# Kernel tuning notes

Measured on AMD Instinct MI355X. Metric: run time of the kernel, lower is better.

The kernel has to match this reference:

```python
import jax, jax.numpy as jnp
import numpy as np

B, S, D = 8, 1024, 1024      # batch, seq_len, inp_dim
H, HD = 8, 64                # head_num, head_dim
HID = H * HD                 # hidden_dim = 512
P = 2 * D                    # p_factor * inp_dim = 2048
K = 4                        # causal conv kernel size
EPS = 1e-6
CAP = 15.0                   # soft cap for i/f gates


def _layernorm(x, g, b):
    mu = jnp.mean(x, -1, keepdims=True)
    var = jnp.var(x, -1, keepdims=True)
    return (x - mu) * jax.lax.rsqrt(var + EPS) * g + b


def _soft_cap(v):
    return CAP * jnp.tanh(v / CAP)


def _causal_conv_feat(x, w, b):
    # Conv1d(1,1,K) applied over the FEATURE axis of each timestep (as in the
    # torch code: x_t.unsqueeze(1) -> (bs,1,P)), causal left pad of K-1.
    L = x.shape[-1]
    xp = jnp.pad(x, ((0, 0), (0, 0), (K - 1, 0)))
    out = b
    for m in range(K):
        out = out + w[m] * xp[..., m:m + L]
    return out


def _forward(x, ln_g, ln_b, mh_g, mh_b, W_up_l, b_up_l, W_up_r, b_up_r,
             W_down, b_down, conv_w, conv_b, W_skip, b_skip, W_i, b_i,
             W_f, b_f, W_o, b_o, W_q, b_q, W_k, b_k, W_v, b_v):
    Bs, Sl, _ = x.shape
    xn = _layernorm(x, ln_g, ln_b)
    x_t = xn @ W_up_l.T + b_up_l                      # (B,S,P)
    r_t = xn @ W_up_r.T + b_up_r                      # (B,S,HID)
    x_c = jax.nn.silu(_causal_conv_feat(x_t, conv_w, conv_b))
    x_skip = x_c @ W_skip.T + b_skip                  # (B,S,HID)
    q = (x_c @ W_q.T + b_q).reshape(Bs, Sl, H, HD)
    k = (x_c @ W_k.T + b_k).reshape(Bs, Sl, H, HD) / float(np.sqrt(HD))
    v = (x_t @ W_v.T + b_v).reshape(Bs, Sl, H, HD)
    i_pre = _soft_cap(x_c @ W_i.T + b_i)              # (B,S,H)
    f_pre = _soft_cap(x_c @ W_f.T + b_f)              # (B,S,H)
    o = jax.nn.sigmoid(x_t @ W_o.T + b_o)             # (B,S,HID)

    def step(carry, inp):
        c, n, m = carry
        qt, kt, vt, it, ft = inp
        m_t = jnp.maximum(ft + m, it)
        ie = jnp.exp(it - m_t)
        fe = jnp.exp(ft - m_t + m)
        c = fe[:, :, None, None] * c + ie[:, :, None, None] * jnp.einsum('bhd,bhe->bhde', vt, kt)
        n = fe[:, :, None] * n + ie[:, :, None] * kt
        num = jnp.einsum('bhde,bhe->bhd', c, qt)
        den = jnp.maximum(jnp.sum(n * qt, -1, keepdims=True), 1.0)
        return (c, n, m_t), num / den

    c0 = jnp.zeros((Bs, H, HD, HD), x.dtype)
    n0 = jnp.ones((Bs, H, HD), x.dtype)
    m0 = jnp.zeros((Bs, H), x.dtype)
    seq = tuple(jnp.moveaxis(a, 1, 0) for a in (q, k, v, i_pre, f_pre))
    _, hs = jax.lax.scan(step, (c0, n0, m0), seq)     # hs: (S,B,H,HD)
    h = o * jnp.moveaxis(hs, 0, 1).reshape(Bs, Sl, HID)
    hn = _layernorm(h.reshape(Bs, Sl, H, HD), mh_g, mh_b).reshape(Bs, Sl, HID)
    out = (hn + x_skip) * jax.nn.silu(r_t)
    return out @ W_down.T + b_down + x


def setup_inputs() -> dict:
    key = jax.random.key(0)
    ks = jax.random.split(key, 16)

    def w(kk, shape):
        return jax.random.normal(kk, shape, jnp.float32) / np.sqrt(shape[-1]).astype(np.float32)

    return {
        'x': jax.random.normal(ks[0], (B, S, D), jnp.float32),
        'ln_g': jnp.ones((D,), jnp.float32), 'ln_b': jnp.zeros((D,), jnp.float32),
        'mh_g': jnp.ones((H, HD), jnp.float32), 'mh_b': jnp.zeros((H, HD), jnp.float32),
        'W_up_l': w(ks[1], (P, D)), 'b_up_l': jnp.zeros((P,), jnp.float32),
        'W_up_r': w(ks[2], (HID, D)), 'b_up_r': jnp.zeros((HID,), jnp.float32),
        'W_down': w(ks[3], (D, HID)), 'b_down': jnp.zeros((D,), jnp.float32),
        'conv_w': jax.random.normal(ks[4], (K,), jnp.float32) * 0.3,
        'conv_b': jnp.zeros((), jnp.float32),
        'W_skip': w(ks[5], (HID, P)), 'b_skip': jnp.zeros((HID,), jnp.float32),
        'W_i': w(ks[6], (H, P)), 'b_i': jnp.zeros((H,), jnp.float32),
        'W_f': w(ks[7], (H, P)), 'b_f': jnp.zeros((H,), jnp.float32),
        'W_o': w(ks[8], (HID, P)), 'b_o': jnp.zeros((HID,), jnp.float32),
        'W_q': w(ks[9], (HID, P)), 'b_q': jnp.zeros((HID,), jnp.float32),
        'W_k': w(ks[10], (HID, P)), 'b_k': jnp.zeros((HID,), jnp.float32),
        'W_v': w(ks[11], (HID, P)), 'b_v': jnp.zeros((HID,), jnp.float32),
    }


def reference(x, ln_g, ln_b, mh_g, mh_b, W_up_l, b_up_l, W_up_r, b_up_r,
              W_down, b_down, conv_w, conv_b, W_skip, b_skip, W_i, b_i,
              W_f, b_f, W_o, b_o, W_q, b_q, W_k, b_k, W_v, b_v):
    return _forward(x, ln_g, ln_b, mh_g, mh_b, W_up_l, b_up_l, W_up_r, b_up_r,
                    W_down, b_down, conv_w, conv_b, W_skip, b_skip, W_i, b_i,
                    W_f, b_f, W_o, b_o, W_q, b_q, W_k, b_k, W_v, b_v)
```

## Files before the change

kernel.cpp:

```cpp
#include <hip/hip_runtime.h>
#include <hip/hip_bf16.h>
#include <math.h>

#define Bq 8
#define Sq 1024
#define Dq 1024
#define Hq 8
#define HDq 64
#define HIDq 512
#define Pq 2048
#define EPSq 1e-6f
#define CAPq 15.0f
#define NCq 16
#define CLq 64
#define LDST 40
#define ARENA (128 * LDST)
#define GEMM_SMEM_BYTES (2 * 4 * ARENA * 2)

typedef __attribute__((ext_vector_type(8))) short short8;
typedef __attribute__((ext_vector_type(4))) float f32x4v;
typedef __hip_bfloat16 bf16;

__device__ inline void split2(float v, bf16& h, bf16& l) {
  h = __float2bfloat16(v);
  l = __float2bfloat16(v - __bfloat162float(h));
}

__global__ __launch_bounds__(256) void cvtw_all(
    const float* __restrict__ s0, const float* __restrict__ s1,
    const float* __restrict__ s2, const float* __restrict__ s3,
    const float* __restrict__ s4, const float* __restrict__ s5,
    const float* __restrict__ s6, const float* __restrict__ s7,
    bf16* __restrict__ hi, bf16* __restrict__ lo)
{
  int u = blockIdx.x * 256 + threadIdx.x;
  const float* src; int segBase;
  if      (u <  524288) { src = s0; segBase = 0;       }
  else if (u <  655360) { src = s1; segBase = 524288;  }
  else if (u <  917504) { src = s2; segBase = 655360;  }
  else if (u < 1179648) { src = s3; segBase = 917504;  }
  else if (u < 1441792) { src = s4; segBase = 1179648; }
  else if (u < 1703936) { src = s5; segBase = 1441792; }
  else if (u < 1966080) { src = s6; segBase = 1703936; }
  else                  { src = s7; segBase = 1966080; }
  float4 v = ((const float4*)src)[u - segBase];
  size_t o = (size_t)u * 4;
  bf16 h, l;
  split2(v.x, h, l); hi[o+0] = h; lo[o+0] = l;
  split2(v.y, h, l); hi[o+1] = h; lo[o+1] = l;
  split2(v.z, h, l); hi[o+2] = h; lo[o+2] = l;
  split2(v.w, h, l); hi[o+3] = h; lo[o+3] = l;
}

__global__ __launch_bounds__(256) void ln_kernel(const float* __restrict__ x,
    const float* __restrict__ g, const float* __restrict__ b,
    bf16* __restrict__ yh, bf16* __restrict__ yl)
{
  int row = blockIdx.x;
  int tid = threadIdx.x;
  const float* xr = x + (size_t)row * Dq;
  float v[4]; float s = 0.f, s2 = 0.f;
  #pragma unroll
  for (int i = 0; i < 4; i++) { v[i] = xr[tid + 256*i]; s += v[i]; s2 += v[i]*v[i]; }
  #pragma unroll
  for (int mm = 32; mm > 0; mm >>= 1) { s += __shfl_xor(s, mm, 64); s2 += __shfl_xor(s2, mm, 64); }
  __shared__ float rs[4], rs2[4];
  int lane = tid & 63, wave = tid >> 6;
  if (lane == 0) { rs[wave] = s; rs2[wave] = s2; }
  __syncthreads();
  s  = rs[0] + rs[1] + rs[2] + rs[3];
  s2 = rs2[0] + rs2[1] + rs2[2] + rs2[3];
  float mu  = s * (1.f / Dq);
  float var = s2 * (1.f / Dq) - mu * mu;
  float r = rsqrtf(var + EPSq);
  #pragma unroll
  for (int i = 0; i < 4; i++) {
    int c = tid + 256*i;
    float y = (v[i] - mu) * r * g[c] + b[c];
    bf16 h, l; split2(y, h, l);
    yh[(size_t)row * Dq + c] = h;
    yl[(size_t)row * Dq + c] = l;
  }
}

__global__ __launch_bounds__(256) void gemm_x3(
    const bf16* __restrict__ Ahi, const bf16* __restrict__ Alo,
    const bf16* __restrict__ Whi, const bf16* __restrict__ Wlo,
    int Kd, int start1, int start2, const float* __restrict__ resid,
    const float* bias0, float* f0, bf16* h0, bf16* l0, int w0, float sc0, int a0,
    const float* bias1, float* f1, bf16* h1, bf16* l1, int w1, float sc1, int a1,
    const float* bias2, float* f2, bf16* h2, bf16* l2, int w2, float sc2, int a2)
{
  extern __shared__ short smem[];
  int tid = threadIdx.x;
  int lane = tid & 63, wave = tid >> 6;
  int wr = wave >> 1, wc = wave & 1;
  int rowBase = blockIdx.y * 128;
  int colBase = blockIdx.x * 128;

  int sk  = (tid & 3) * 8;
  int sr0 = tid >> 2;
  int sr1 = 64 + sr0;

  const short* Ahg = (const short*)Ahi + (size_t)rowBase * Kd;
  const short* Alg = (const short*)Alo + (size_t)rowBase * Kd;
  const short* Bhg = (const short*)Whi + (size_t)colBase * Kd;
  const short* Blg = (const short*)Wlo + (size_t)colBase * Kd;

  f32x4v acc[4][4];
  #pragma unroll
  for (int i = 0; i < 4; i++)
    #pragma unroll
    for (int j = 0; j < 4; j++) acc[i][j] = (f32x4v){0.f, 0.f, 0.f, 0.f};

  int fk = (lane >> 4) * 8;
  int fr = lane & 15;
  int nk = Kd >> 5;

  short8 ah0, ah1, al0, al1, bh0, bh1, bl0, bl1;

#define LOAD_TILE(k0) do {                                                    \
    size_t o0 = (size_t)sr0 * Kd + (k0) + sk;                                 \
    size_t o1 = (size_t)sr1 * Kd + (k0) + sk;                                 \
    ah0 = *(const short8*)(Ahg + o0); ah1 = *(const short8*)(Ahg + o1);       \
    al0 = *(const short8*)(Alg + o0); al1 = *(const short8*)(Alg + o1);       \
    bh0 = *(const short8*)(Bhg + o0); bh1 = *(const short8*)(Bhg + o1);       \
    bl0 = *(const short8*)(Blg + o0); bl1 = *(const short8*)(Blg + o1);       \
  } while (0)

#define STORE_TILE(S) do {                                                    \
    *(short8*)&(S)[0*ARENA + sr0*LDST + sk] = ah0;                            \
    *(short8*)&(S)[0*ARENA + sr1*LDST + sk] = ah1;                            \
    *(short8*)&(S)[1*ARENA + sr0*LDST + sk] = al0;                            \
    *(short8*)&(S)[1*ARENA + sr1*LDST + sk] = al1;                            \
    *(short8*)&(S)[2*ARENA + sr0*LDST + sk] = bh0;                            \
    *(short8*)&(S)[2*ARENA + sr1*LDST + sk] = bh1;                            \
    *(short8*)&(S)[3*ARENA + sr0*LDST + sk] = bl0;                            \
    *(short8*)&(S)[3*ARENA + sr1*LDST + sk] = bl1;                            \
  } while (0)

  LOAD_TILE(0);
  STORE_TILE(smem);
  __syncthreads();

  for (int t = 0; t < nk; ++t) {
    const short* C = smem + (t & 1) * (4 * ARENA);
    short* Nx      = smem + ((t + 1) & 1) * (4 * ARENA);
    bool pf = (t + 1 < nk);
    if (pf) LOAD_TILE((size_t)(t + 1) << 5);

    short8 afh[4], afl[4], bfh[4], bfl[4];
    #pragma unroll
    for (int mi = 0; mi < 4; mi++) {
      afh[mi] = *(const short8*)&C[0*ARENA + (wr * 64 + mi * 16 + fr) * LDST + fk];
      afl[mi] = *(const short8*)&C[1*ARENA + (wr * 64 + mi * 16 + fr) * LDST + fk];
    }
    #pragma unroll
    for (int ni = 0; ni < 4; ni++) {
      bfh[ni] = *(const short8*)&C[2*ARENA + (wc * 64 + ni * 16 + fr) * LDST + fk];
      bfl[ni] = *(const short8*)&C[3*ARENA + (wc * 64 + ni * 16 + fr) * LDST + fk];
    }
    #pragma unroll
    for (int mi = 0; mi < 4; mi++)
      #pragma unroll
      for (int ni = 0; ni < 4; ni++)
        acc[mi][ni] = __builtin_amdgcn_mfma_f32_16x16x32_bf16(afh[mi], bfh[ni], acc[mi][ni], 0, 0, 0);
    #pragma unroll
    for (int mi = 0; mi < 4; mi++)
      #pragma unroll
      for (int ni = 0; ni < 4; ni++)
        acc[mi][ni] = __builtin_amdgcn_mfma_f32_16x16x32_bf16(afh[mi], bfl[ni], acc[mi][ni], 0, 0, 0);
    #pragma unroll
    for (int mi = 0; mi < 4; mi++)
      #pragma unroll
      for (int ni = 0; ni < 4; ni++)
        acc[mi][ni] = __builtin_amdgcn_mfma_f32_16x16x32_bf16(afl[mi], bfh[ni], acc[mi][ni], 0, 0, 0);

    __builtin_amdgcn_sched_barrier(0);
    if (pf) STORE_TILE(Nx);
    __syncthreads();
  }
#undef LOAD_TILE
#undef STORE_TILE

  const float* bias; float* fOut; bf16* hOut; bf16* lOut; int segStart, segW; float sscale; int sact;
  if (colBase >= start2)      { bias=bias2; fOut=f2; hOut=h2; lOut=l2; segStart=start2; segW=w2; sscale=sc2; sact=a2; }
  else if (colBase >= start1) { bias=bias1; fOut=f1; hOut=h1; lOut=l1; segStart=start1; segW=w1; sscale=sc1; sact=a1; }
  else                        { bias=bias0; fOut=f0; hOut=h0; lOut=l0; segStart=0;      segW=w0; sscale=sc0; sact=a0; }

  int cr = (lane >> 4) * 4;
  int cc = lane & 15;
  #pragma unroll
  for (int mi = 0; mi < 4; mi++) {
    #pragma unroll
    for (int ni = 0; ni < 4; ni++) {
      int col  = colBase + wc * 64 + ni * 16 + cc;
      int colL = col - segStart;
      float bv = bias[colL];
      #pragma unroll
      for (int j = 0; j < 4; j++) {
        int row = rowBase + wr * 64 + mi * 16 + cr + j;
        float val = (acc[mi][ni][j] + bv) * sscale;
        if (sact) val = 1.f / (1.f + expf(-val));
        if (resid && segStart == 0) val += resid[(size_t)row * segW + colL];
        size_t oidx = (size_t)row * segW + colL;
        if (fOut) fOut[oidx] = val;
        if (hOut) {
          bf16 h, l; split2(val, h, l);
          hOut[oidx] = h; lOut[oidx] = l;
        }
      }
    }
  }
}

__global__ __launch_bounds__(256) void conv_kernel(const bf16* __restrict__ xth,
    const bf16* __restrict__ xtl, const float* __restrict__ cw,
    const float* __restrict__ cb, bf16* __restrict__ xch, bf16* __restrict__ xcl,
    int total)
{
  int idx = blockIdx.x * 256 + threadIdx.x;
  if (idx >= total) return;
  int p = idx & (Pq - 1);
  #define XT(i) (__bfloat162float(xth[i]) + __bfloat162float(xtl[i]))
  float acc = cb[0] + cw[3] * XT(idx);
  if (p >= 1) acc += cw[2] * XT(idx - 1);
  if (p >= 2) acc += cw[1] * XT(idx - 2);
  if (p >= 3) acc += cw[0] * XT(idx - 3);
  #undef XT
  float y = acc / (1.f + expf(-acc));
  bf16 h, l; split2(y, h, l);
  xch[idx] = h; xcl[idx] = l;
}

__global__ __launch_bounds__(256) void ifk_kernel(const bf16* __restrict__ xch,
    const bf16* __restrict__ xcl,
    const float* __restrict__ Wi, const float* __restrict__ bi,
    const float* __restrict__ Wf, const float* __restrict__ bf_,
    float* __restrict__ ip, float* __restrict__ fp)
{
  int row = blockIdx.x;
  int lane = threadIdx.x & 63, wave = threadIdx.x >> 6;
  size_t rb = (size_t)row * Pq;
  for (int oi = wave; oi < 16; oi += 4) {
    int hh = oi & 7;
    const float* Wrow = (oi < 8) ? (Wi + (size_t)hh * Pq) : (Wf + (size_t)hh * Pq);
    float s = 0.f;
    for (int j = lane; j < Pq; j += 64)
      s += (__bfloat162float(xch[rb + j]) + __bfloat162float(xcl[rb + j])) * Wrow[j];
    #pragma unroll
    for (int mm = 32; mm > 0; mm >>= 1) s += __shfl_xor(s, mm, 64);
    if (lane == 0) {
      float val = s + ((oi < 8) ? bi[hh] : bf_[hh]);
      val = CAPq * tanhf(val / CAPq);
      if (oi < 8) ip[(size_t)row * Hq + hh] = val;
      else        fp[(size_t)row * Hq + hh] = val;
    }
  }
}

__global__ __launch_bounds__(256) void chunkA_kernel(const float* __restrict__ k,
    const float* __restrict__ v, const float* __restrict__ ip,
    const float* __restrict__ fp, float* __restrict__ bg,
    float* __restrict__ FcMc, float* __restrict__ kvg, float* __restrict__ ksumg)
{
  int blk = blockIdx.x;
  int bh = blk >> 4, c = blk & 15;
  int b = bh >> 3, hh = bh & 7;
  int tid = threadIdx.x, lane = tid & 63, wave = tid >> 6;

  __shared__ float sK[64][64], sV[64][64], sW[64];

  size_t base = (size_t)b * Sq * 512 + (size_t)hh * 64 + (size_t)c * CLq * 512;
  #pragma unroll 4
  for (int i = 0; i < 16; i++) {
    int t = wave * 16 + i;
    sK[t][lane] = k[base + (size_t)t * 512 + lane];
    sV[t][lane] = v[base + (size_t)t * 512 + lane];
  }
  if (tid < 64) {
    size_t ifb = ((size_t)b * Sq + c * CLq + tid) * Hq + hh;
    float fv = fp[ifb], iv = ip[ifb];
    float cf = fv;
    #pragma unroll
    for (int off = 1; off < 64; off <<= 1) {
      float t2 = __shfl_up(cf, off, 64);
      if (lane >= off) cf += t2;
    }
    float bs = iv - cf;
    float mx = bs;
    #pragma unroll
    for (int off = 1; off < 64; off <<= 1) {
      float t2 = __shfl_up(mx, off, 64);
      if (lane >= off) mx = fmaxf(mx, t2);
    }
    float Mc = __shfl(mx, 63, 64);
    bg[(size_t)blk * 64 + tid] = bs;
    sW[tid] = expf(bs - Mc);
    if (tid == 63) { FcMc[blk*2] = cf; FcMc[blk*2+1] = Mc; }
  }
  __syncthreads();
  float acc[16];
  #pragma unroll
  for (int j = 0; j < 16; j++) acc[j] = 0.f;
  for (int s = 0; s < 64; s++) {
    float wv = sW[s] * sV[s][lane];
    #pragma unroll
    for (int j = 0; j < 16; j++) acc[j] += wv * sK[s][wave*16+j];
  }
  float* kvp = kvg + (size_t)blk * 4096 + lane * 64 + wave * 16;
  #pragma unroll
  for (int j = 0; j < 16; j++) kvp[j] = acc[j];
  if (tid < 64) {
    float a = 0.f;
    for (int s = 0; s < 64; s++) a += sW[s] * sK[s][tid];
    ksumg[(size_t)blk * 64 + tid] = a;
  }
}

__global__ __launch_bounds__(256) void chunkB_kernel(const float* __restrict__ kvg,
    const float* __restrict__ ksumg, const float* __restrict__ FcMc,
    float* __restrict__ boundC, float* __restrict__ boundN, float* __restrict__ boundM)
{
  int bh = blockIdx.x;
  int tid = threadIdx.x, lane = tid & 63, wave = tid >> 6;
  float C[16];
  #pragma unroll
  for (int j = 0; j < 16; j++) C[j] = 0.f;
  float ne = 1.0f, m = 0.f;
  for (int c = 0; c < NCq; c++) {
    size_t blk = (size_t)bh * NCq + c;
    float* bC = boundC + blk * 4096 + lane * 64 + wave * 16;
    #pragma unroll
    for (int j = 0; j < 16; j++) bC[j] = C[j];
    if (wave == 0) boundN[blk * 64 + lane] = ne;
    if (tid == 0)  boundM[blk] = m;
    float Fc = FcMc[blk * 2], Mc = FcMc[blk * 2 + 1];
    float mm = fmaxf(m, Mc);
    float a1 = expf(m - mm), a2 = expf(Mc - mm);
    const float* kv = kvg + blk * 4096 + lane * 64 + wave * 16;
    #pragma unroll
    for (int j = 0; j < 16; j++) C[j] = a1 * C[j] + a2 * kv[j];
    ne = a1 * ne + a2 * ksumg[blk * 64 + lane];
    m = Fc + mm;
  }
}

__global__ __launch_bounds__(256) void chunkC_kernel(const float* q,
    const float* __restrict__ k, const float* __restrict__ v,
    const float* __restrict__ bg, const float* __restrict__ boundC,
    const float* __restrict__ boundN, const float* __restrict__ boundM,
    float* hs)
{
  int blk = blockIdx.x;
  int bh = blk >> 4, c = blk & 15;
  int b = bh >> 3, hh = bh & 7;
  int tid = threadIdx.x, lane = tid & 63, wave = tid >> 6;

  __shared__ float sQ[64][65], sKV[64][65], sS[64][65];
  __shared__ float sB[64], sMr[64], sNin[64];

  size_t base = (size_t)b * Sq * 512 + (size_t)hh * 64 + (size_t)c * CLq * 512;
  #pragma unroll 4
  for (int i = 0; i < 16; i++) {
    int t = wave * 16 + i;
    sQ[t][lane]  = q[base + (size_t)t * 512 + lane];
    sKV[t][lane] = k[base + (size_t)t * 512 + lane];
  }
  float m_in = boundM[blk];
  if (tid < 64) {
    float bs = bg[(size_t)blk * 64 + tid];
    float mx = bs;
    #pragma unroll
    for (int off = 1; off < 64; off <<= 1) {
      float t2 = __shfl_up(mx, off, 64);
      if (lane >= off) mx = fmaxf(mx, t2);
    }
    sB[tid]   = bs;
    sMr[tid]  = fmaxf(m_in, mx);
    sNin[tid] = boundN[(size_t)blk * 64 + tid];
  }
  __syncthreads();

  {
    int t = lane;
    float acc[16];
    #pragma unroll
    for (int j = 0; j < 16; j++) acc[j] = 0.f;
    for (int d = 0; d < 64; d++) {
      float qv = sQ[t][d];
      #pragma unroll
      for (int j = 0; j < 16; j++) acc[j] += qv * sKV[wave*16+j][d];
    }
    float Mr = sMr[t];
    #pragma unroll
    for (int j = 0; j < 16; j++) {
      int s = wave * 16 + j;
      float w = (s <= t) ? expf(sB[s] - Mr) : 0.f;
      sS[t][s] = w * acc[j];
    }
  }
  __syncthreads();
  #pragma unroll 4
  for (int i = 0; i < 16; i++) {
    int t = wave * 16 + i;
    sKV[t][lane] = v[base + (size_t)t * 512 + lane];
  }
  __syncthreads();

  {
    int t = lane;
    float Mr = sMr[t];
    float bfac = expf(m_in - Mr);
    float den = 0.f;
    for (int d = 0; d < 64; d++) den += sNin[d] * sQ[t][d];
    den *= bfac;
    float num[16];
    #pragma unroll
    for (int j = 0; j < 16; j++) num[j] = 0.f;
    const float* Crow = boundC + (size_t)blk * 4096;
    for (int e = 0; e < 64; e++) {
      float qv = sQ[t][e];
      #pragma unroll
      for (int j = 0; j < 16; j++)
        num[j] += Crow[(size_t)(wave*16+j) * 64 + e] * qv;
    }
    #pragma unroll
    for (int j = 0; j < 16; j++) num[j] *= bfac;
    for (int s = 0; s < 64; s++) {
      float ws = sS[t][s];
      den += ws;
      #pragma unroll
      for (int j = 0; j < 16; j++) num[j] += ws * sKV[s][wave*16+j];
    }
    den = fmaxf(den, 1.0f);
    float o[16];
    #pragma unroll
    for (int j = 0; j < 16; j++) o[j] = num[j] / den;
    float* hp = hs + base + (size_t)t * 512 + wave * 16;
    #pragma unroll
    for (int j4 = 0; j4 < 4; j4++)
      ((float4*)hp)[j4] = ((float4*)o)[j4];
  }
}

__global__ __launch_bounds__(256) void epi_kernel(const float* __restrict__ hsv,
    const float* __restrict__ ov, const float* __restrict__ xs,
    const float* __restrict__ rt, const float* __restrict__ mg,
    const float* __restrict__ mb, bf16* __restrict__ pdh, bf16* __restrict__ pdl)
{
  int tid = threadIdx.x;
  int lane = tid & 63, wave = tid >> 6;
  size_t row = (size_t)blockIdx.x * 4 + wave;
  int hh = (int)(row & 7);
  size_t idx = row * 64 + lane;
  float hv = ov[idx] * hsv[idx];
  float s = hv, s2 = hv * hv;
  #pragma unroll
  for (int mm = 32; mm > 0; mm >>= 1) { s += __shfl_xor(s, mm, 64); s2 += __shfl_xor(s2, mm, 64); }
  float mu  = s * (1.f / 64.f);
  float var = s2 * (1.f / 64.f) - mu * mu;
  float r = rsqrtf(var + EPSq);
  float hn = (hv - mu) * r * mg[hh * 64 + lane] + mb[hh * 64 + lane];
  float rv = rt[idx];
  float y = (hn + xs[idx]) * (rv / (1.f + expf(-rv)));
  bf16 h, l; split2(y, h, l);
  pdh[idx] = h; pdl[idx] = l;
}

extern "C" void kernel_launch(void* const* d_in, const int* in_sizes, int n_in,
                              void* d_out, int out_size, void* d_ws, size_t ws_size,
                              hipStream_t stream)
{
  const float* x      = (const float*)d_in[0];
  const float* ln_g   = (const float*)d_in[1];
  const float* ln_b   = (const float*)d_in[2];
  const float* mh_g   = (const float*)d_in[3];
  const float* mh_b   = (const float*)d_in[4];
  const float* W_up_l = (const float*)d_in[5];
  const float* b_up_l = (const float*)d_in[6];
  const float* W_up_r = (const float*)d_in[7];
  const float* b_up_r = (const float*)d_in[8];
  const float* W_down = (const float*)d_in[9];
  const float* b_down = (const float*)d_in[10];
  const float* conv_w = (const float*)d_in[11];
  const float* conv_b = (const float*)d_in[12];
  const float* W_skip = (const float*)d_in[13];
  const float* b_skip = (const float*)d_in[14];
  const float* W_i    = (const float*)d_in[15];
  const float* b_i    = (const float*)d_in[16];
  const float* W_f    = (const float*)d_in[17];
  const float* b_f    = (const float*)d_in[18];
  const float* W_o    = (const float*)d_in[19];
  const float* b_o    = (const float*)d_in[20];
  const float* W_q    = (const float*)d_in[21];
  const float* b_q    = (const float*)d_in[22];
  const float* W_k    = (const float*)d_in[23];
  const float* b_k    = (const float*)d_in[24];
  const float* W_v    = (const float*)d_in[25];
  const float* b_v    = (const float*)d_in[26];
  float* out = (float*)d_out;

  const size_t MB = 1u << 20;
  if (ws_size < 193 * MB) return;

  static bool attrSet = false;
  if (!attrSet) {
    (void)hipFuncSetAttribute(reinterpret_cast<const void*>(gemm_x3),
                              hipFuncAttributeMaxDynamicSharedMemorySize,
                              GEMM_SMEM_BYTES);
    attrSet = true;
  }

  char* base = (char*)d_ws;
  bf16* whi = (bf16*)base;
  bf16* wlo = (bf16*)(base + 16*MB);
  bf16* xnh = (bf16*)(base + 32*MB);
  bf16* xnl = (bf16*)(base + 48*MB);
  bf16* xth = (bf16*)(base + 64*MB);
  bf16* xtl = (bf16*)(base + 96*MB);
  bf16* xch = (bf16*)(base + 128*MB);
  bf16* xcl = (bf16*)(base + 160*MB);
  float* vb  = (float*)(base + 32*MB);
  float* ob  = (float*)(base + 48*MB);
  float* xs  = (float*)(base + 64*MB);
  float* qb  = (float*)(base + 80*MB);
  float* kb  = (float*)(base + 96*MB);
  bf16*  pdh = (bf16*)(base + 112*MB);
  bf16*  pdl = (bf16*)(base + 120*MB);
  float* kvg    = (float*)(base + 128*MB);
  float* boundC = (float*)(base + 144*MB);
  float* bg     = (float*)(base + 160*MB);
  float* ksumg  = (float*)(base + 160*MB + 256*1024);
  float* boundN = (float*)(base + 160*MB + 512*1024);
  float* FcMc   = (float*)(base + 160*MB + 768*1024);
  float* boundM = (float*)(base + 160*MB + 776*1024);
  float* ip  = (float*)(base + 192*MB);
  float* fpb = (float*)(base + 192*MB + 256*1024);
  float* rt  = out;
  float* hsb = qb;

  const int Mrows = Bq * Sq;
  const int BIG = 1 << 30;

  cvtw_all<<<dim3(8192), dim3(256), 0, stream>>>(
      W_up_l, W_up_r, W_v, W_o, W_skip, W_q, W_k, W_down, whi, wlo);

  ln_kernel<<<dim3(Mrows), dim3(256), 0, stream>>>(x, ln_g, ln_b, xnh, xnl);

  gemm_x3<<<dim3(20, 64), dim3(256), GEMM_SMEM_BYTES, stream>>>(
      xnh, xnl, whi, wlo, 1024, 2048, BIG, nullptr,
      b_up_l, nullptr, xth, xtl, 2048, 1.f, 0,
      b_up_r, rt, nullptr, nullptr, 512, 1.f, 0,
      nullptr, nullptr, nullptr, nullptr, 1, 1.f, 0);

  gemm_x3<<<dim3(8, 64), dim3(256), GEMM_SMEM_BYTES, stream>>>(
      xth, xtl, whi + 2621440, wlo + 2621440, 2048, 512, BIG, nullptr,
      b_v, vb, nullptr, nullptr, 512, 1.f, 0,
      b_o, ob, nullptr, nullptr, 512, 1.f, 1,
      nullptr, nullptr, nullptr, nullptr, 1, 1.f, 0);

  int convTotal = Mrows * Pq;
  conv_kernel<<<dim3(convTotal / 256), dim3(256), 0, stream>>>(
      xth, xtl, conv_w, conv_b, xch, xcl, convTotal);

  gemm_x3<<<dim3(12, 64), dim3(256), GEMM_SMEM_BYTES, stream>>>(
      xch, xcl, whi + 4718592, wlo + 4718592, 2048, 512, 1024, nullptr,
      b_skip, xs, nullptr, nullptr, 512, 1.f, 0,
      b_q, qb, nullptr, nullptr, 512, 1.f, 0,
      b_k, kb, nullptr, nullptr, 512, 0.125f, 0);

  ifk_kernel<<<dim3(Mrows), dim3(256), 0, stream>>>(
      xch, xcl, W_i, b_i, W_f, b_f, ip, fpb);

  chunkA_kernel<<<dim3(Bq * Hq * NCq), dim3(256), 0, stream>>>(
      kb, vb, ip, fpb, bg, FcMc, kvg, ksumg);
  chunkB_kernel<<<dim3(Bq * Hq), dim3(256), 0, stream>>>(
      kvg, ksumg, FcMc, boundC, boundN, boundM);
  chunkC_kernel<<<dim3(Bq * Hq * NCq), dim3(256), 0, stream>>>(
      qb, kb, vb, bg, boundC, boundN, boundM, hsb);

  epi_kernel<<<dim3(Mrows * Hq / 4), dim3(256), 0, stream>>>(
      hsb, ob, xs, rt, mh_g, mh_b, pdh, pdl);

  gemm_x3<<<dim3(8, 64), dim3(256), GEMM_SMEM_BYTES, stream>>>(
      pdh, pdl, whi + 7864320, wlo + 7864320, 512, BIG, BIG, x,
      b_down, out, nullptr, nullptr, 1024, 1.f, 0,
      nullptr, nullptr, nullptr, nullptr, 1, 1.f, 0,
      nullptr, nullptr, nullptr, nullptr, 1, 1.f, 0);
}
```

Before: 1.005 ms.

## Remap GEMM blocks across XCDs and vectorize conv and i/f gate kernels

The GEMM kernel now remaps its flat block index so that consecutive logical tiles land on the same XCD chunk (blocks are strided by 8), aiming for better L2 reuse of A/W tiles. The conv kernel processes 8 features per thread with 16-byte vector loads and stores plus a halo load. The i/f gate kernel reads activations and weights with vectorized loads. The remap assumes the block count is divisible by 8, which holds for the current grids.

```diff
diff --git a/kernel.cpp b/kernel.cpp
--- a/kernel.cpp
+++ b/kernel.cpp
@@ -24,6 +24,11 @@
 __device__ inline void split2(float v, bf16& h, bf16& l) {
   h = __float2bfloat16(v);
   l = __float2bfloat16(v - __bfloat162float(h));
+}
+
+__device__ inline float bfs2f(short s) {
+  bf16 t = *(const bf16*)&s;
+  return __bfloat162float(t);
 }
 
 __global__ __launch_bounds__(256) void cvtw_all(
@@ -95,8 +100,15 @@
   int tid = threadIdx.x;
   int lane = tid & 63, wave = tid >> 6;
   int wr = wave >> 1, wc = wave & 1;
-  int rowBase = blockIdx.y * 128;
-  int colBase = blockIdx.x * 128;
+
+  int gx = gridDim.x;
+  int flat = blockIdx.y * gx + blockIdx.x;
+  int nb = gx * gridDim.y;
+  int chunk = nb >> 3;
+  int nid = (flat & 7) * chunk + (flat >> 3);
+  int col = nid % gx, row = nid / gx;
+  int rowBase = row * 128;
+  int colBase = col * 128;
 
   int sk  = (tid & 3) * 8;
   int sr0 = tid >> 2;
@@ -194,16 +206,16 @@
   for (int mi = 0; mi < 4; mi++) {
     #pragma unroll
     for (int ni = 0; ni < 4; ni++) {
-      int col  = colBase + wc * 64 + ni * 16 + cc;
-      int colL = col - segStart;
+      int colO  = colBase + wc * 64 + ni * 16 + cc;
+      int colL = colO - segStart;
       float bv = bias[colL];
       #pragma unroll
       for (int j = 0; j < 4; j++) {
-        int row = rowBase + wr * 64 + mi * 16 + cr + j;
+        int rowO = rowBase + wr * 64 + mi * 16 + cr + j;
         float val = (acc[mi][ni][j] + bv) * sscale;
         if (sact) val = 1.f / (1.f + expf(-val));
-        if (resid && segStart == 0) val += resid[(size_t)row * segW + colL];
-        size_t oidx = (size_t)row * segW + colL;
+        if (resid && segStart == 0) val += resid[(size_t)rowO * segW + colL];
+        size_t oidx = (size_t)rowO * segW + colL;
         if (fOut) fOut[oidx] = val;
         if (hOut) {
           bf16 h, l; split2(val, h, l);
@@ -217,20 +229,40 @@
 __global__ __launch_bounds__(256) void conv_kernel(const bf16* __restrict__ xth,
     const bf16* __restrict__ xtl, const float* __restrict__ cw,
     const float* __restrict__ cb, bf16* __restrict__ xch, bf16* __restrict__ xcl,
-    int total)
-{
-  int idx = blockIdx.x * 256 + threadIdx.x;
-  if (idx >= total) return;
-  int p = idx & (Pq - 1);
-  #define XT(i) (__bfloat162float(xth[i]) + __bfloat162float(xtl[i]))
-  float acc = cb[0] + cw[3] * XT(idx);
-  if (p >= 1) acc += cw[2] * XT(idx - 1);
-  if (p >= 2) acc += cw[1] * XT(idx - 2);
-  if (p >= 3) acc += cw[0] * XT(idx - 3);
-  #undef XT
-  float y = acc / (1.f + expf(-acc));
-  bf16 h, l; split2(y, h, l);
-  xch[idx] = h; xcl[idx] = l;
+    int total8)
+{
+  int u = blockIdx.x * 256 + threadIdx.x;
+  if (u >= total8) return;
+  size_t idx = (size_t)u * 8;
+  int p0 = (int)(idx & (Pq - 1));
+  const short* hp = (const short*)xth + idx;
+  const short* lp = (const short*)xtl + idx;
+  short8 ch = *(const short8*)hp;
+  short8 cl = *(const short8*)lp;
+  float xv[11];
+  #pragma unroll
+  for (int j = 0; j < 8; j++) xv[3 + j] = bfs2f(ch[j]) + bfs2f(cl[j]);
+  if (p0 > 0) {
+    short8 ph = *(const short8*)(hp - 8);
+    short8 pl = *(const short8*)(lp - 8);
+    xv[0] = bfs2f(ph[5]) + bfs2f(pl[5]);
+    xv[1] = bfs2f(ph[6]) + bfs2f(pl[6]);
+    xv[2] = bfs2f(ph[7]) + bfs2f(pl[7]);
+  } else {
+    xv[0] = xv[1] = xv[2] = 0.f;
+  }
+  float w0 = cw[0], w1 = cw[1], w2 = cw[2], w3 = cw[3], bb = cb[0];
+  short8 oh, ol;
+  #pragma unroll
+  for (int j = 0; j < 8; j++) {
+    float acc = bb + w3 * xv[j + 3] + w2 * xv[j + 2] + w1 * xv[j + 1] + w0 * xv[j];
+    float y = acc / (1.f + expf(-acc));
+    bf16 h, l; split2(y, h, l);
+    oh[j] = *(const short*)&h;
+    ol[j] = *(const short*)&l;
+  }
+  *(short8*)((short*)xch + idx) = oh;
+  *(short8*)((short*)xcl + idx) = ol;
 }
 
 __global__ __launch_bounds__(256) void ifk_kernel(const bf16* __restrict__ xch,
@@ -242,12 +274,26 @@
   int row = blockIdx.x;
   int lane = threadIdx.x & 63, wave = threadIdx.x >> 6;
   size_t rb = (size_t)row * Pq;
+  const short* xh = (const short*)xch + rb;
+  const short* xl = (const short*)xcl + rb;
   for (int oi = wave; oi < 16; oi += 4) {
     int hh = oi & 7;
     const float* Wrow = (oi < 8) ? (Wi + (size_t)hh * Pq) : (Wf + (size_t)hh * Pq);
     float s = 0.f;
-    for (int j = lane; j < Pq; j += 64)
-      s += (__bfloat162float(xch[rb + j]) + __bfloat162float(xcl[rb + j])) * Wrow[j];
+    for (int j0 = lane * 8; j0 < Pq; j0 += 512) {
+      short8 hv = *(const short8*)(xh + j0);
+      short8 lv = *(const short8*)(xl + j0);
+      float4 wa = *(const float4*)(Wrow + j0);
+      float4 wb = *(const float4*)(Wrow + j0 + 4);
+      s += (bfs2f(hv[0]) + bfs2f(lv[0])) * wa.x;
+      s += (bfs2f(hv[1]) + bfs2f(lv[1])) * wa.y;
+      s += (bfs2f(hv[2]) + bfs2f(lv[2])) * wa.z;
+      s += (bfs2f(hv[3]) + bfs2f(lv[3])) * wa.w;
+      s += (bfs2f(hv[4]) + bfs2f(lv[4])) * wb.x;
+      s += (bfs2f(hv[5]) + bfs2f(lv[5])) * wb.y;
+      s += (bfs2f(hv[6]) + bfs2f(lv[6])) * wb.z;
+      s += (bfs2f(hv[7]) + bfs2f(lv[7])) * wb.w;
+    }
     #pragma unroll
     for (int mm = 32; mm > 0; mm >>= 1) s += __shfl_xor(s, mm, 64);
     if (lane == 0) {
@@ -560,9 +606,9 @@
       b_o, ob, nullptr, nullptr, 512, 1.f, 1,
       nullptr, nullptr, nullptr, nullptr, 1, 1.f, 0);
 
-  int convTotal = Mrows * Pq;
-  conv_kernel<<<dim3(convTotal / 256), dim3(256), 0, stream>>>(
-      xth, xtl, conv_w, conv_b, xch, xcl, convTotal);
+  int convTotal8 = Mrows * Pq / 8;
+  conv_kernel<<<dim3(convTotal8 / 256), dim3(256), 0, stream>>>(
+      xth, xtl, conv_w, conv_b, xch, xcl, convTotal8);
 
   gemm_x3<<<dim3(12, 64), dim3(256), GEMM_SMEM_BYTES, stream>>>(
       xch, xcl, whi + 4718592, wlo + 4718592, 2048, 512, 1024, nullptr,
```

Measured after the change: 905.3 us. 9.9% less time.
